# Optimization experiments

Hardware: AMD Instinct MI355X
Metric: run time of the kernel (lower is better)

The kernel has to match this reference:

```python
import jax, jax.numpy as jnp
import numpy as np

GAMMA0 = 1.0


def patch_to_image(patches):
    # patches: [b, n_patch, patch_dim, 1, T] -> image [b, 1, g*p, g*p, T]
    b, n_patch, patch_dim, _, T = patches.shape
    p = int(patch_dim ** 0.5)
    g = int(n_patch ** 0.5)
    img = patches[:, :, :, 0, :]                      # [b, n_patch, p*p, T]
    img = jnp.transpose(img, (0, 3, 1, 2))            # [b, T, n_patch, p*p]
    img = img.reshape(b, T, g, g, p, p)
    img = jnp.transpose(img, (0, 1, 2, 4, 3, 5)).reshape(b, T, 1, g * p, g * p)
    return jnp.transpose(img, (0, 2, 3, 4, 1))        # [b, 1, g*p, g*p, T]


def setup_inputs() -> dict:
    key = jax.random.key(0)
    k0, k1, k2, k3, k4, k5 = jax.random.split(key, 6)
    X = jax.random.normal(k0, (32, 64, 300, 1, 50), dtype=jnp.float32)
    U = jax.random.normal(k1, (32, 1, 40, 1, 50), dtype=jnp.float32)
    x0 = jax.random.normal(k2, (32, 64, 300, 1), dtype=jnp.float32)
    # dictionaries, column-normalized like torch's norm(dim=2, keepdim=True)
    A = jax.random.uniform(k3, (300, 300), dtype=jnp.float32)
    A = A / jnp.linalg.norm(A, axis=0, keepdims=True)
    B = jax.random.uniform(k4, (300, 40), dtype=jnp.float32)
    B = B / jnp.linalg.norm(B, axis=0, keepdims=True)
    C = jax.random.uniform(k5, (256, 300), dtype=jnp.float32)
    C = C / jnp.linalg.norm(C, axis=0, keepdims=True)
    return {"X": X, "U": U, "x0": x0, "A": A, "B": B, "C": C}


def reference(X, U, x0, A, B, C):
    # X: [b, P, 300, 1, T]  U: [b, 1, 40, 1, T]  x0: [b, P, 300, 1]
    # Prediction x_hat_t = A @ x_{t-1}, with x_{-1} = x0 (vectorized over T)
    x_prev = jnp.concatenate([x0[..., None], X[..., :-1]], axis=-1)   # [b,P,300,1,T]
    X_pred = jnp.einsum('ij,bpjut->bpiut', A, x_prev)                 # [b,P,300,1,T]
    # Reconstruction recon_t = C @ x_t, assembled into frames
    recon = jnp.einsum('dj,bpjut->bpdut', C, X)                       # [b,P,256,1,T]
    vid_recon = patch_to_image(recon)                                 # [b,1,128,128,T]
    # Cause state: gamma_t * sum_patches |x_t|
    Bu = jnp.einsum('ij,bqjut->bqiut', B, U)                          # [b,1,300,1,T]
    gamma = GAMMA0 * (1.0 + jnp.exp(-Bu)) / 2.0
    X_U = gamma * jnp.sum(jnp.abs(X), axis=1, keepdims=True)          # [b,1,300,1,T]
    return (vid_recon, X_pred, X_U)
```

## Files before the change

### kernel.cpp

```cpp
#include <hip/hip_runtime.h>

typedef _Float16 half8 __attribute__((ext_vector_type(8)));
typedef _Float16 half4v __attribute__((ext_vector_type(4)));
typedef float f32x4 __attribute__((ext_vector_type(4)));
typedef unsigned long long ull;

#define OFF_PRED 26214400
#define OFF_XU   56934400

__global__ void build_M(const float* __restrict__ A, const float* __restrict__ C,
                        _Float16* __restrict__ M) {
    int idx = blockIdx.x * 256 + threadIdx.x;
    if (idx >= 640 * 320) return;
    int e    = idx & 7;
    int lane = (idx >> 3) & 63;
    int fs   = idx >> 9;
    int mt = fs / 10, ks = fs % 10;
    int m = mt * 16 + (lane & 15);
    int k = ks * 32 + (lane >> 4) * 8 + e;
    float v = 0.f;
    if (k < 300) {
        if (m < 256) v = C[m * 300 + k];
        else if (m < 556) v = A[(m - 256) * 300 + k];
    }
    M[idx] = (_Float16)v;
}

__global__ __launch_bounds__(256, 2) void gemm_main(
    const float* __restrict__ X, const float* __restrict__ x0,
    const _Float16* __restrict__ M, float* __restrict__ out)
{
    __shared__ _Float16 lds[2 * 64 * 320];
    char* ldsb = (char*)lds;
    const int sw = ((blockIdx.x & 7) << 8) + (blockIdx.x >> 3);
    const int bpp = sw >> 1, mhalf = sw & 1;
    const int bp0 = bpp * 2;
    const int tid = threadIdx.x;

    const int wave = tid >> 6, lane = tid & 63;
    const int lr = lane & 15, lg = lane >> 4;
    const int g = wave;

    const _Float16* Mw = M + (mhalf * 4 + g) * 50 * 512 + lane * 8;

    half8 pf[5];
    #pragma unroll
    for (int j = 0; j < 5; j++) pf[j] = *(const half8*)(Mw + (j * 10) * 512);

    #pragma unroll
    for (int tau = 0; tau < 2; tau++) {
        char* lb = ldsb + tau * 40960;
        if (tid < 255) {
            int row = tid / 5, c = tid % 5;
            *(ull*)(lb + row * 640 + ((600 + c * 8) ^ ((row & 7) << 4))) = 0ULL;
        }
        #pragma unroll
        for (int u = 0; u < 5; u++) {
            int i = tid + u * 256;
            if (i < 1040) *(ull*)(lb + 51 * 640 + i * 8) = 0ULL;
        }
    }
    if (tid < 150) {
        int tau = tid / 75, c = tid - tau * 75;
        f32x4 v = *(const f32x4*)(x0 + (bp0 + tau) * 300 + c * 4);
        half4v h4 = { (_Float16)v.x, (_Float16)v.y, (_Float16)v.z, (_Float16)v.w };
        *(half4v*)(ldsb + tau * 40960 + c * 8) = h4;
    }
    #pragma unroll
    for (int u = 0; u < 15; u++) {
        int i = tid + u * 256;
        if (i < 3750) {
            int tau = i / 1875, rem = i - tau * 1875;
            int tp = rem % 25, jq = rem / 25;
            const float* s = X + (bp0 + tau) * 15000 + jq * 200 + tp * 2;
            float2 v0 = *(const float2*)(s);
            float2 v1 = *(const float2*)(s + 50);
            float2 v2 = *(const float2*)(s + 100);
            float2 v3 = *(const float2*)(s + 150);
            char* lb = ldsb + tau * 40960;
            int r1 = tp * 2 + 1, r2 = tp * 2 + 2;
            half4v h1 = { (_Float16)v0.x, (_Float16)v1.x, (_Float16)v2.x, (_Float16)v3.x };
            half4v h2 = { (_Float16)v0.y, (_Float16)v1.y, (_Float16)v2.y, (_Float16)v3.y };
            *(half4v*)(lb + r1 * 640 + ((jq * 8) ^ ((r1 & 7) << 4))) = h1;
            *(half4v*)(lb + r2 * 640 + ((jq * 8) ^ ((r2 & 7) << 4))) = h2;
        }
    }
    __syncthreads();

    f32x4 acc0[5][4], acc1[5][4];
    #pragma unroll
    for (int j = 0; j < 5; j++)
        #pragma unroll
        for (int nt = 0; nt < 4; nt++) {
            acc0[j][nt] = (f32x4){0.f, 0.f, 0.f, 0.f};
            acc1[j][nt] = (f32x4){0.f, 0.f, 0.f, 0.f};
        }

    #define LDSA(TB, nt, ks) (*(const half8*)(ldsb + (TB) + ((nt) * 16 + lr) * 640 + \
                             (((ks) * 64 + lg * 16) ^ ((lr & 7) << 4))))

    #pragma unroll
    for (int ks = 0; ks < 10; ks++) {
        half8 bf0, bf1, bf2, bf3, bf4;
        if (ks == 0) {
            bf0 = pf[0]; bf1 = pf[1]; bf2 = pf[2]; bf3 = pf[3]; bf4 = pf[4];
        } else {
            bf0 = *(const half8*)(Mw + (0 * 10 + ks) * 512);
            bf1 = *(const half8*)(Mw + (1 * 10 + ks) * 512);
            bf2 = *(const half8*)(Mw + (2 * 10 + ks) * 512);
            bf3 = *(const half8*)(Mw + (3 * 10 + ks) * 512);
            bf4 = *(const half8*)(Mw + (4 * 10 + ks) * 512);
        }
        #pragma unroll
        for (int nt = 0; nt < 4; nt++) {
            half8 a = LDSA(0, nt, ks);
            acc0[0][nt] = __builtin_amdgcn_mfma_f32_16x16x32_f16(a, bf0, acc0[0][nt], 0, 0, 0);
            acc0[1][nt] = __builtin_amdgcn_mfma_f32_16x16x32_f16(a, bf1, acc0[1][nt], 0, 0, 0);
            acc0[2][nt] = __builtin_amdgcn_mfma_f32_16x16x32_f16(a, bf2, acc0[2][nt], 0, 0, 0);
            acc0[3][nt] = __builtin_amdgcn_mfma_f32_16x16x32_f16(a, bf3, acc0[3][nt], 0, 0, 0);
            acc0[4][nt] = __builtin_amdgcn_mfma_f32_16x16x32_f16(a, bf4, acc0[4][nt], 0, 0, 0);
        }
        #pragma unroll
        for (int nt = 0; nt < 4; nt++) {
            half8 a = LDSA(40960, nt, ks);
            acc1[0][nt] = __builtin_amdgcn_mfma_f32_16x16x32_f16(a, bf0, acc1[0][nt], 0, 0, 0);
            acc1[1][nt] = __builtin_amdgcn_mfma_f32_16x16x32_f16(a, bf1, acc1[1][nt], 0, 0, 0);
            acc1[2][nt] = __builtin_amdgcn_mfma_f32_16x16x32_f16(a, bf2, acc1[2][nt], 0, 0, 0);
            acc1[3][nt] = __builtin_amdgcn_mfma_f32_16x16x32_f16(a, bf3, acc1[3][nt], 0, 0, 0);
            acc1[4][nt] = __builtin_amdgcn_mfma_f32_16x16x32_f16(a, bf4, acc1[4][nt], 0, 0, 0);
        }
    }
    #undef LDSA

#define EPILOGUE(ACC, BP) { \
    const int b_ = (BP) >> 6, p_ = (BP) & 63; \
    const int gr_ = p_ >> 3, gc_ = p_ & 7; \
    _Pragma("unroll") \
    for (int j = 0; j < 5; j++) { \
        int colm = mhalf * 320 + g * 80 + j * 16 + lr; \
        if (colm < 256) { \
            int base = b_ * 819200 + ((gr_ * 16 + (colm >> 4)) * 128 + gc_ * 16 + (colm & 15)) * 50; \
            _Pragma("unroll") \
            for (int nt = 0; nt < 4; nt++) { \
                int t0 = nt * 16 + lg * 4; \
                if (t0 == 0) { \
                    out[base + 0] = ACC[j][0][1]; \
                    out[base + 1] = ACC[j][0][2]; \
                    out[base + 2] = ACC[j][0][3]; \
                } else if (t0 <= 46) { \
                    f32x4 v = ACC[j][nt]; \
                    __builtin_memcpy(&out[base + t0 - 1], &v, 16); \
                } else if (t0 == 48) { \
                    out[base + 47] = ACC[j][nt][0]; \
                    out[base + 48] = ACC[j][nt][1]; \
                    out[base + 49] = ACC[j][nt][2]; \
                } \
            } \
        } else if (colm < 556) { \
            int base = OFF_PRED + ((BP) * 300 + (colm - 256)) * 50; \
            _Pragma("unroll") \
            for (int nt = 0; nt < 4; nt++) { \
                int t0 = nt * 16 + lg * 4; \
                if (t0 <= 46) { \
                    f32x4 v = ACC[j][nt]; \
                    __builtin_memcpy(&out[base + t0], &v, 16); \
                } else if (t0 == 48) { \
                    out[base + 48] = ACC[j][nt][0]; \
                    out[base + 49] = ACC[j][nt][1]; \
                } \
            } \
        } \
    } }

    EPILOGUE(acc0, bp0);
    EPILOGUE(acc1, bp0 + 1);
#undef EPILOGUE
}

__global__ void xu_kernel(const float* __restrict__ X, const float* __restrict__ U,
                          const float* __restrict__ B, float* __restrict__ out) {
    int id = blockIdx.x * 256 + threadIdx.x;
    if (id >= 480000) return;
    int t = id % 50;
    int i = (id / 50) % 300;
    int b = id / 15000;
    const float* xp = X + b * 960000 + i * 50 + t;
    float s = 0.f;
    #pragma unroll 8
    for (int pp = 0; pp < 64; pp++) s += fabsf(xp[pp * 15000]);
    float bu = 0.f;
    const float* up = U + b * 2000 + t;
    const float* Bp = B + i * 40;
    #pragma unroll 8
    for (int q = 0; q < 40; q++) bu += Bp[q] * up[q * 50];
    out[OFF_XU + id] = 0.5f * (1.f + expf(-bu)) * s;
}

extern "C" void kernel_launch(void* const* d_in, const int* in_sizes, int n_in,
                              void* d_out, int out_size, void* d_ws, size_t ws_size,
                              hipStream_t stream) {
    const float* X  = (const float*)d_in[0];
    const float* U  = (const float*)d_in[1];
    const float* x0 = (const float*)d_in[2];
    const float* A  = (const float*)d_in[3];
    const float* B  = (const float*)d_in[4];
    const float* C  = (const float*)d_in[5];
    float* out = (float*)d_out;
    _Float16* M = (_Float16*)d_ws;

    build_M<<<800, 256, 0, stream>>>(A, C, M);
    gemm_main<<<2048, 256, 0, stream>>>(X, x0, M, out);
    xu_kernel<<<1875, 256, 0, stream>>>(X, U, B, out);
}
```

Measured before the change: 125.1 us.

## Switch GEMM operands from fp16 to fp8 MFMA with unswizzled LDS layout

```diff
diff --git a/kernel.cpp b/kernel.cpp
--- a/kernel.cpp
+++ b/kernel.cpp
@@ -1,37 +1,46 @@
 #include <hip/hip_runtime.h>
 
-typedef _Float16 half8 __attribute__((ext_vector_type(8)));
-typedef _Float16 half4v __attribute__((ext_vector_type(4)));
 typedef float f32x4 __attribute__((ext_vector_type(4)));
 typedef unsigned long long ull;
 
 #define OFF_PRED 26214400
 #define OFF_XU   56934400
+#define LROW 328
+#define BUFSZ (64 * LROW)
+
+__device__ inline unsigned pack4_fp8(float a, float b, float c, float d) {
+    int r = __builtin_amdgcn_cvt_pk_fp8_f32(a, b, 0, false);
+    r = __builtin_amdgcn_cvt_pk_fp8_f32(c, d, r, true);
+    return (unsigned)r;
+}
 
 __global__ void build_M(const float* __restrict__ A, const float* __restrict__ C,
-                        _Float16* __restrict__ M) {
+                        unsigned* __restrict__ M) {
     int idx = blockIdx.x * 256 + threadIdx.x;
-    if (idx >= 640 * 320) return;
-    int e    = idx & 7;
-    int lane = (idx >> 3) & 63;
-    int fs   = idx >> 9;
+    if (idx >= 51200) return;
+    int d = idx * 4;
+    int e0 = d & 7, lane = (d >> 3) & 63, fs = d >> 9;
     int mt = fs / 10, ks = fs % 10;
     int m = mt * 16 + (lane & 15);
-    int k = ks * 32 + (lane >> 4) * 8 + e;
-    float v = 0.f;
-    if (k < 300) {
-        if (m < 256) v = C[m * 300 + k];
-        else if (m < 556) v = A[(m - 256) * 300 + k];
-    }
-    M[idx] = (_Float16)v;
+    int k = ks * 32 + (lane >> 4) * 8 + e0;
+    float f0 = 0.f, f1 = 0.f, f2 = 0.f, f3 = 0.f;
+    const float* src = nullptr;
+    if (m < 256) src = C + m * 300;
+    else if (m < 556) src = A + (m - 256) * 300;
+    if (src) {
+        if (k + 0 < 300) f0 = src[k + 0];
+        if (k + 1 < 300) f1 = src[k + 1];
+        if (k + 2 < 300) f2 = src[k + 2];
+        if (k + 3 < 300) f3 = src[k + 3];
+    }
+    M[idx] = pack4_fp8(f0, f1, f2, f3);
 }
 
 __global__ __launch_bounds__(256, 2) void gemm_main(
     const float* __restrict__ X, const float* __restrict__ x0,
-    const _Float16* __restrict__ M, float* __restrict__ out)
+    const char* __restrict__ M, float* __restrict__ out)
 {
-    __shared__ _Float16 lds[2 * 64 * 320];
-    char* ldsb = (char*)lds;
+    __shared__ char ldsb[2 * BUFSZ];
     const int sw = ((blockIdx.x & 7) << 8) + (blockIdx.x >> 3);
     const int bpp = sw >> 1, mhalf = sw & 1;
     const int bp0 = bpp * 2;
@@ -41,30 +50,33 @@
     const int lr = lane & 15, lg = lane >> 4;
     const int g = wave;
 
-    const _Float16* Mw = M + (mhalf * 4 + g) * 50 * 512 + lane * 8;
-
-    half8 pf[5];
-    #pragma unroll
-    for (int j = 0; j < 5; j++) pf[j] = *(const half8*)(Mw + (j * 10) * 512);
-
-    #pragma unroll
-    for (int tau = 0; tau < 2; tau++) {
-        char* lb = ldsb + tau * 40960;
-        if (tid < 255) {
-            int row = tid / 5, c = tid % 5;
-            *(ull*)(lb + row * 640 + ((600 + c * 8) ^ ((row & 7) << 4))) = 0ULL;
-        }
-        #pragma unroll
-        for (int u = 0; u < 5; u++) {
-            int i = tid + u * 256;
-            if (i < 1040) *(ull*)(lb + 51 * 640 + i * 8) = 0ULL;
+    const char* Mw = M + ((mhalf * 4 + g) * 5 * 10) * 512 + lane * 8;
+
+    long long pf[5];
+    #pragma unroll
+    for (int j = 0; j < 5; j++) pf[j] = *(const long long*)(Mw + (j * 10) * 512);
+
+    #pragma unroll
+    for (int u = 0; u < 2; u++) {
+        int i = tid + u * 256;
+        if (i < 357) {
+            int row = i / 7, c = i % 7;
+            *(unsigned*)(ldsb + row * LROW + 300 + c * 4) = 0u;
+            *(unsigned*)(ldsb + BUFSZ + row * LROW + 300 + c * 4) = 0u;
+        }
+    }
+    #pragma unroll
+    for (int u = 0; u < 3; u++) {
+        int i = tid + u * 256;
+        if (i < 533) {
+            *(ull*)(ldsb + 16728 + i * 8) = 0ULL;
+            *(ull*)(ldsb + BUFSZ + 16728 + i * 8) = 0ULL;
         }
     }
     if (tid < 150) {
         int tau = tid / 75, c = tid - tau * 75;
         f32x4 v = *(const f32x4*)(x0 + (bp0 + tau) * 300 + c * 4);
-        half4v h4 = { (_Float16)v.x, (_Float16)v.y, (_Float16)v.z, (_Float16)v.w };
-        *(half4v*)(ldsb + tau * 40960 + c * 8) = h4;
+        *(unsigned*)(ldsb + tau * BUFSZ + c * 4) = pack4_fp8(v.x, v.y, v.z, v.w);
     }
     #pragma unroll
     for (int u = 0; u < 15; u++) {
@@ -77,12 +89,9 @@
             float2 v1 = *(const float2*)(s + 50);
             float2 v2 = *(const float2*)(s + 100);
             float2 v3 = *(const float2*)(s + 150);
-            char* lb = ldsb + tau * 40960;
-            int r1 = tp * 2 + 1, r2 = tp * 2 + 2;
-            half4v h1 = { (_Float16)v0.x, (_Float16)v1.x, (_Float16)v2.x, (_Float16)v3.x };
-            half4v h2 = { (_Float16)v0.y, (_Float16)v1.y, (_Float16)v2.y, (_Float16)v3.y };
-            *(half4v*)(lb + r1 * 640 + ((jq * 8) ^ ((r1 & 7) << 4))) = h1;
-            *(half4v*)(lb + r2 * 640 + ((jq * 8) ^ ((r2 & 7) << 4))) = h2;
+            char* lb = ldsb + tau * BUFSZ;
+            *(unsigned*)(lb + (tp * 2 + 1) * LROW + jq * 4) = pack4_fp8(v0.x, v1.x, v2.x, v3.x);
+            *(unsigned*)(lb + (tp * 2 + 2) * LROW + jq * 4) = pack4_fp8(v0.y, v1.y, v2.y, v3.y);
         }
     }
     __syncthreads();
@@ -96,38 +105,38 @@
             acc1[j][nt] = (f32x4){0.f, 0.f, 0.f, 0.f};
         }
 
-    #define LDSA(TB, nt, ks) (*(const half8*)(ldsb + (TB) + ((nt) * 16 + lr) * 640 + \
-                             (((ks) * 64 + lg * 16) ^ ((lr & 7) << 4))))
+    #define LDSA(TB, nt, ks) (*(const long long*)(ldsb + (TB) + ((nt) * 16 + lr) * LROW + \
+                             (ks) * 32 + lg * 8))
 
     #pragma unroll
     for (int ks = 0; ks < 10; ks++) {
-        half8 bf0, bf1, bf2, bf3, bf4;
+        long long bf0, bf1, bf2, bf3, bf4;
         if (ks == 0) {
             bf0 = pf[0]; bf1 = pf[1]; bf2 = pf[2]; bf3 = pf[3]; bf4 = pf[4];
         } else {
-            bf0 = *(const half8*)(Mw + (0 * 10 + ks) * 512);
-            bf1 = *(const half8*)(Mw + (1 * 10 + ks) * 512);
-            bf2 = *(const half8*)(Mw + (2 * 10 + ks) * 512);
-            bf3 = *(const half8*)(Mw + (3 * 10 + ks) * 512);
-            bf4 = *(const half8*)(Mw + (4 * 10 + ks) * 512);
+            bf0 = *(const long long*)(Mw + (0 * 10 + ks) * 512);
+            bf1 = *(const long long*)(Mw + (1 * 10 + ks) * 512);
+            bf2 = *(const long long*)(Mw + (2 * 10 + ks) * 512);
+            bf3 = *(const long long*)(Mw + (3 * 10 + ks) * 512);
+            bf4 = *(const long long*)(Mw + (4 * 10 + ks) * 512);
         }
         #pragma unroll
         for (int nt = 0; nt < 4; nt++) {
-            half8 a = LDSA(0, nt, ks);
-            acc0[0][nt] = __builtin_amdgcn_mfma_f32_16x16x32_f16(a, bf0, acc0[0][nt], 0, 0, 0);
-            acc0[1][nt] = __builtin_amdgcn_mfma_f32_16x16x32_f16(a, bf1, acc0[1][nt], 0, 0, 0);
-            acc0[2][nt] = __builtin_amdgcn_mfma_f32_16x16x32_f16(a, bf2, acc0[2][nt], 0, 0, 0);
-            acc0[3][nt] = __builtin_amdgcn_mfma_f32_16x16x32_f16(a, bf3, acc0[3][nt], 0, 0, 0);
-            acc0[4][nt] = __builtin_amdgcn_mfma_f32_16x16x32_f16(a, bf4, acc0[4][nt], 0, 0, 0);
+            long long a = LDSA(0, nt, ks);
+            acc0[0][nt] = __builtin_amdgcn_mfma_f32_16x16x32_fp8_fp8(a, bf0, acc0[0][nt], 0, 0, 0);
+            acc0[1][nt] = __builtin_amdgcn_mfma_f32_16x16x32_fp8_fp8(a, bf1, acc0[1][nt], 0, 0, 0);
+            acc0[2][nt] = __builtin_amdgcn_mfma_f32_16x16x32_fp8_fp8(a, bf2, acc0[2][nt], 0, 0, 0);
+            acc0[3][nt] = __builtin_amdgcn_mfma_f32_16x16x32_fp8_fp8(a, bf3, acc0[3][nt], 0, 0, 0);
+            acc0[4][nt] = __builtin_amdgcn_mfma_f32_16x16x32_fp8_fp8(a, bf4, acc0[4][nt], 0, 0, 0);
         }
         #pragma unroll
         for (int nt = 0; nt < 4; nt++) {
-            half8 a = LDSA(40960, nt, ks);
-            acc1[0][nt] = __builtin_amdgcn_mfma_f32_16x16x32_f16(a, bf0, acc1[0][nt], 0, 0, 0);
-            acc1[1][nt] = __builtin_amdgcn_mfma_f32_16x16x32_f16(a, bf1, acc1[1][nt], 0, 0, 0);
-            acc1[2][nt] = __builtin_amdgcn_mfma_f32_16x16x32_f16(a, bf2, acc1[2][nt], 0, 0, 0);
-            acc1[3][nt] = __builtin_amdgcn_mfma_f32_16x16x32_f16(a, bf3, acc1[3][nt], 0, 0, 0);
-            acc1[4][nt] = __builtin_amdgcn_mfma_f32_16x16x32_f16(a, bf4, acc1[4][nt], 0, 0, 0);
+            long long a = LDSA(BUFSZ, nt, ks);
+            acc1[0][nt] = __builtin_amdgcn_mfma_f32_16x16x32_fp8_fp8(a, bf0, acc1[0][nt], 0, 0, 0);
+            acc1[1][nt] = __builtin_amdgcn_mfma_f32_16x16x32_fp8_fp8(a, bf1, acc1[1][nt], 0, 0, 0);
+            acc1[2][nt] = __builtin_amdgcn_mfma_f32_16x16x32_fp8_fp8(a, bf2, acc1[2][nt], 0, 0, 0);
+            acc1[3][nt] = __builtin_amdgcn_mfma_f32_16x16x32_fp8_fp8(a, bf3, acc1[3][nt], 0, 0, 0);
+            acc1[4][nt] = __builtin_amdgcn_mfma_f32_16x16x32_fp8_fp8(a, bf4, acc1[4][nt], 0, 0, 0);
         }
     }
     #undef LDSA
@@ -206,9 +215,9 @@
     const float* B  = (const float*)d_in[4];
     const float* C  = (const float*)d_in[5];
     float* out = (float*)d_out;
-    _Float16* M = (_Float16*)d_ws;
-
-    build_M<<<800, 256, 0, stream>>>(A, C, M);
-    gemm_main<<<2048, 256, 0, stream>>>(X, x0, M, out);
+    unsigned* M = (unsigned*)d_ws;
+
+    build_M<<<200, 256, 0, stream>>>(A, C, M);
+    gemm_main<<<2048, 256, 0, stream>>>(X, x0, (const char*)M, out);
     xu_kernel<<<1875, 256, 0, stream>>>(X, U, B, out);
 }
```

Result: faster. 120.3 us (-3.9%).
